# Kernel tuning notes

Measured on AMD Instinct MI355X. Metric: run time of the kernel, lower is better.

Reference implementation:

```python
import jax, jax.numpy as jnp
import numpy as np

N_NODES = 100000
N_EDGES = 1600000
NFEAT, NHID, NCLASS = 128, 64, 40
DROPOUT_P = 0.5


def setup_inputs() -> dict:
    key = jax.random.key(0)
    k1, k2, k3, k4 = jax.random.split(key, 4)
    inputs = jax.random.normal(k1, (N_NODES, NFEAT), dtype=jnp.float32)
    edge_index = jax.random.randint(k2, (2, N_EDGES), 0, N_NODES, dtype=jnp.int64)
    # Glorot-uniform-ish init like torch Linear / PyG GCNConv
    lim1 = float(np.sqrt(6.0 / (NFEAT + NHID)))
    lim2 = float(np.sqrt(6.0 / (NHID + NCLASS)))
    W1 = jax.random.uniform(k3, (NFEAT, NHID), minval=-lim1, maxval=lim1, dtype=jnp.float32)
    W2 = jax.random.uniform(k4, (NHID, NCLASS), minval=-lim2, maxval=lim2, dtype=jnp.float32)
    b1 = jnp.zeros((NHID,), dtype=jnp.float32)
    b2 = jnp.zeros((NCLASS,), dtype=jnp.float32)
    return {"inputs": inputs, "edge_index": edge_index, "W1": W1, "b1": b1, "W2": W2, "b2": b2}


def _gcn_conv(x, W, b, src, dst, norm, n_nodes):
    # PyG GCNConv: out[i] = sum_{j->i} norm_ij * (x W)[j] + b
    xw = x @ W                              # [N, out_dim]
    msg = xw[src] * norm[:, None]           # [E+N, out_dim] gather + scale
    out = jax.ops.segment_sum(msg, dst, num_segments=n_nodes)  # scatter-add
    return out + b


def reference(inputs, edge_index, W1, b1, W2, b2):
    n = inputs.shape[0]
    loops = jnp.arange(n, dtype=edge_index.dtype)
    src = jnp.concatenate([edge_index[0], loops])   # add self-loops
    dst = jnp.concatenate([edge_index[1], loops])
    # symmetric normalization D^{-1/2} (A+I) D^{-1/2}
    deg = jax.ops.segment_sum(jnp.ones_like(src, dtype=inputs.dtype), dst, num_segments=n)
    dis = jnp.where(deg > 0, jax.lax.rsqrt(jnp.maximum(deg, 1.0)), 0.0)
    norm = dis[src] * dis[dst]
    # dropout on inputs (training mode, fixed key for determinism)
    keep = jax.random.bernoulli(jax.random.key(42), 1.0 - DROPOUT_P, inputs.shape)
    x = jnp.where(keep, inputs / (1.0 - DROPOUT_P), 0.0)
    h = jax.nn.relu(_gcn_conv(x, W1, b1, src, dst, norm, n))
    out = _gcn_conv(h, W2, b2, src, dst, norm, n)
    return out
```

## Files before the change

kernel.cpp:

```cpp
#include <hip/hip_runtime.h>

#define NF 128
#define NH 64
#define NC 40
#define BSHIFT 10
#define NB 98
#define BIN_T 8192

typedef __attribute__((ext_vector_type(8))) short short8;
typedef __attribute__((ext_vector_type(4))) float float4v;

__device__ __forceinline__ unsigned rotl32(unsigned v, int s) { return (v << s) | (v >> (32 - s)); }

__device__ __forceinline__ unsigned short f2bf(float f) {
  unsigned u = __float_as_uint(f);
  return (unsigned short)((u + 0x7FFFu + ((u >> 16) & 1u)) >> 16);
}
__device__ __forceinline__ float bf2f(unsigned short b) {
  return __uint_as_float(((unsigned)b) << 16);
}

__device__ __forceinline__ unsigned threefry_bits(unsigned idx) {
  const unsigned k0 = 0u, k1 = 42u;
  const unsigned k2x = 0u ^ 42u ^ 0x1BD11BDAu;
  unsigned x0 = 0u, x1 = idx;
  x0 += k0; x1 += k1;
  x0 += x1; x1 = rotl32(x1, 13); x1 ^= x0;
  x0 += x1; x1 = rotl32(x1, 15); x1 ^= x0;
  x0 += x1; x1 = rotl32(x1, 26); x1 ^= x0;
  x0 += x1; x1 = rotl32(x1, 6);  x1 ^= x0;
  x0 += k1; x1 += k2x + 1u;
  x0 += x1; x1 = rotl32(x1, 17); x1 ^= x0;
  x0 += x1; x1 = rotl32(x1, 29); x1 ^= x0;
  x0 += x1; x1 = rotl32(x1, 16); x1 ^= x0;
  x0 += x1; x1 = rotl32(x1, 24); x1 ^= x0;
  x0 += k2x; x1 += k0 + 2u;
  x0 += x1; x1 = rotl32(x1, 13); x1 ^= x0;
  x0 += x1; x1 = rotl32(x1, 15); x1 ^= x0;
  x0 += x1; x1 = rotl32(x1, 26); x1 ^= x0;
  x0 += x1; x1 = rotl32(x1, 6);  x1 ^= x0;
  x0 += k0; x1 += k1 + 3u;
  x0 += x1; x1 = rotl32(x1, 17); x1 ^= x0;
  x0 += x1; x1 = rotl32(x1, 29); x1 ^= x0;
  x0 += x1; x1 = rotl32(x1, 16); x1 ^= x0;
  x0 += x1; x1 = rotl32(x1, 24); x1 ^= x0;
  x0 += k1; x1 += k2x + 4u;
  x0 += x1; x1 = rotl32(x1, 13); x1 ^= x0;
  x0 += x1; x1 = rotl32(x1, 15); x1 ^= x0;
  x0 += x1; x1 = rotl32(x1, 26); x1 ^= x0;
  x0 += x1; x1 = rotl32(x1, 6);  x1 ^= x0;
  x0 += k2x; x1 += k0 + 5u;
  return x0 ^ x1;
}

__global__ __launch_bounds__(256) void k_prep(const float* __restrict__ W1, const float* __restrict__ W2,
                                              unsigned short* __restrict__ Wt1b, unsigned short* __restrict__ Wt2b) {
  int id = blockIdx.x * 256 + threadIdx.x;
  if (id < NF * NH) {
    int k = id >> 6, c = id & 63;
    Wt1b[c * NF + k] = f2bf(W1[id]);
  } else if (id < NF * NH + 48 * NH) {
    int id2 = id - NF * NH;
    int c = id2 >> 6, k = id2 & 63;
    Wt2b[c * NH + k] = (c < NC) ? f2bf(W2[k * NC + c]) : 0;
  }
}

__global__ __launch_bounds__(256) void k_bhist(const int* __restrict__ dst, int* __restrict__ bcnt, int nE) {
  __shared__ int h[NB];
  int t = threadIdx.x;
  if (t < NB) h[t] = 0;
  __syncthreads();
  int stride = gridDim.x * 256;
  for (int e = blockIdx.x * 256 + t; e < nE; e += stride)
    atomicAdd(&h[dst[e] >> BSHIFT], 1);
  __syncthreads();
  if (t < NB && h[t]) atomicAdd(&bcnt[t], h[t]);
}

__global__ __launch_bounds__(128) void k_bscan(const int* __restrict__ bcnt, int* __restrict__ bbase,
                                               int* __restrict__ gcur, int* __restrict__ rp, int n, int nE) {
  int t = threadIdx.x;
  int v = (t < NB) ? bcnt[t] : 0;
  __shared__ int sh[128];
  sh[t] = v; __syncthreads();
  for (int off = 1; off < 128; off <<= 1) {
    int u = (t >= off) ? sh[t - off] : 0; __syncthreads();
    sh[t] += u; __syncthreads();
  }
  int excl = sh[t] - v;
  if (t < NB) { bbase[t] = excl; gcur[t] = excl; }
  if (t == 0) { bbase[NB] = nE; rp[n] = nE; }
}

__global__ __launch_bounds__(256) void k_bin(const int* __restrict__ src, const int* __restrict__ dst,
                                             int* __restrict__ gcur, unsigned* __restrict__ binned, int nE) {
  __shared__ int h[NB];
  __shared__ int off[NB];
  int t = threadIdx.x;
  int b0 = blockIdx.x * BIN_T;
  int b1 = b0 + BIN_T; if (b1 > nE) b1 = nE;
  if (t < NB) h[t] = 0;
  __syncthreads();
  for (int e = b0 + t; e < b1; e += 256)
    atomicAdd(&h[dst[e] >> BSHIFT], 1);
  __syncthreads();
  if (t < NB && h[t] > 0) off[t] = atomicAdd(&gcur[t], h[t]);
  __syncthreads();
  for (int e = b0 + t; e < b1; e += 256) {
    int s = src[e], d = dst[e];
    int p = atomicAdd(&off[d >> BSHIFT], 1);
    binned[p] = ((unsigned)s << BSHIFT) | (unsigned)(d & ((1 << BSHIFT) - 1));
  }
}

__global__ __launch_bounds__(1024) void k_fillb(const unsigned* __restrict__ binned, const int* __restrict__ bbase,
                                                int* __restrict__ rp, float* __restrict__ dis,
                                                int* __restrict__ csrc, int n) {
  __shared__ int hist[1024];
  __shared__ int sbuf[1024];
  int b = blockIdx.x;
  int base = b << BSHIFT;
  int t = threadIdx.x;
  int lo = bbase[b], hi = bbase[b + 1];
  hist[t] = 0;
  __syncthreads();
  for (int e = lo + t; e < hi; e += 1024)
    atomicAdd(&hist[binned[e] & 1023u], 1);
  __syncthreads();
  int v = hist[t];
  sbuf[t] = v; __syncthreads();
  for (int off = 1; off < 1024; off <<= 1) {
    int u = (t >= off) ? sbuf[t - off] : 0; __syncthreads();
    sbuf[t] += u; __syncthreads();
  }
  int excl = sbuf[t] - v;
  if (base + t < n) {
    rp[base + t] = lo + excl;
    dis[base + t] = rsqrtf((float)(v + 1));
  }
  __syncthreads();
  hist[t] = lo + excl;
  __syncthreads();
  for (int e = lo + t; e < hi; e += 1024) {
    unsigned p = binned[e];
    int pos = atomicAdd(&hist[p & 1023u], 1);
    csrc[pos] = (int)(p >> BSHIFT);
  }
}

__global__ __launch_bounds__(256) void k_xw(const float* __restrict__ x, const unsigned short* __restrict__ Wt1b,
                                            const float* __restrict__ dis, unsigned short* __restrict__ y1b, int n) {
  __shared__ unsigned short Ws[NH * 136];
  __shared__ unsigned short xs[16 * 136];
  int t = threadIdx.x;
  int nodeBase = blockIdx.x * 16;
  for (int id = t; id < NH * 16; id += 256) {
    int c = id >> 4, kc = id & 15;
    *(short8*)&Ws[c * 136 + kc * 8] = *(const short8*)&Wt1b[c * NF + kc * 8];
  }
  {
    int nloc = t >> 4, kbase = (t & 15) * 8;
    int ebase = (nodeBase + nloc) * NF + kbase;
    const float4* xp = (const float4*)x;
    float4 a = xp[(ebase >> 2)];
    float4 b = xp[(ebase >> 2) + 1];
    float v[8] = {a.x, a.y, a.z, a.w, b.x, b.y, b.z, b.w};
#pragma unroll
    for (int q = 0; q < 8; ++q) {
      unsigned idx = (unsigned)(ebase + q);
      bool keep = (threefry_bits(idx) & 0x80000000u) == 0u;
      xs[nloc * 136 + kbase + q] = keep ? f2bf(v[q] * 2.0f) : 0;
    }
  }
  __syncthreads();
  int w = t >> 6, lane = t & 63;
  int m = lane & 15, quad = lane >> 4;
  float4v acc = {0.f, 0.f, 0.f, 0.f};
#pragma unroll
  for (int ks = 0; ks < 4; ++ks) {
    short8 a = *(const short8*)&xs[m * 136 + ks * 32 + quad * 8];
    short8 b = *(const short8*)&Ws[(w * 16 + m) * 136 + ks * 32 + quad * 8];
    acc = __builtin_amdgcn_mfma_f32_16x16x32_bf16(a, b, acc, 0, 0, 0);
  }
#pragma unroll
  for (int r = 0; r < 4; ++r) {
    int node = nodeBase + quad * 4 + r;
    y1b[node * NH + w * 16 + m] = f2bf(acc[r] * dis[node]);
  }
}

#define ACC8(u) \
  a0 += __uint_as_float((u).x << 16); \
  a1 += __uint_as_float((u).x & 0xFFFF0000u); \
  a2 += __uint_as_float((u).y << 16); \
  a3 += __uint_as_float((u).y & 0xFFFF0000u); \
  a4 += __uint_as_float((u).z << 16); \
  a5 += __uint_as_float((u).z & 0xFFFF0000u); \
  a6 += __uint_as_float((u).w << 16); \
  a7 += __uint_as_float((u).w & 0xFFFF0000u);

__device__ __forceinline__ unsigned packbf(float lo, float hi) {
  return (unsigned)f2bf(lo) | ((unsigned)f2bf(hi) << 16);
}

__global__ __launch_bounds__(256) void k_agg1(const unsigned short* __restrict__ y1b, const int* __restrict__ rp,
                                              const int* __restrict__ csrc, const float* __restrict__ dis,
                                              const float* __restrict__ b1, unsigned short* __restrict__ gb, int n) {
  int i = blockIdx.x * 32 + (threadIdx.x >> 3);
  if (i >= n) return;
  int fl = (threadIdx.x & 7) << 3;
  const uint4 us = *(const uint4*)&y1b[(i << 6) + fl];
  float a0 = __uint_as_float(us.x << 16);
  float a1 = __uint_as_float(us.x & 0xFFFF0000u);
  float a2 = __uint_as_float(us.y << 16);
  float a3 = __uint_as_float(us.y & 0xFFFF0000u);
  float a4 = __uint_as_float(us.z << 16);
  float a5 = __uint_as_float(us.z & 0xFFFF0000u);
  float a6 = __uint_as_float(us.w << 16);
  float a7 = __uint_as_float(us.w & 0xFFFF0000u);
  int lo = rp[i], hi = rp[i + 1];
  int e = lo;
  int s0, s1, s2, s3;
  if (e + 4 <= hi) { s0 = csrc[e]; s1 = csrc[e + 1]; s2 = csrc[e + 2]; s3 = csrc[e + 3]; }
  for (; e + 8 <= hi; e += 4) {
    uint4 u0 = *(const uint4*)&y1b[(s0 << 6) + fl];
    uint4 u1 = *(const uint4*)&y1b[(s1 << 6) + fl];
    uint4 u2 = *(const uint4*)&y1b[(s2 << 6) + fl];
    uint4 u3 = *(const uint4*)&y1b[(s3 << 6) + fl];
    s0 = csrc[e + 4]; s1 = csrc[e + 5]; s2 = csrc[e + 6]; s3 = csrc[e + 7];
    ACC8(u0) ACC8(u1) ACC8(u2) ACC8(u3)
  }
  if (e + 4 <= hi) {
    uint4 u0 = *(const uint4*)&y1b[(s0 << 6) + fl];
    uint4 u1 = *(const uint4*)&y1b[(s1 << 6) + fl];
    uint4 u2 = *(const uint4*)&y1b[(s2 << 6) + fl];
    uint4 u3 = *(const uint4*)&y1b[(s3 << 6) + fl];
    ACC8(u0) ACC8(u1) ACC8(u2) ACC8(u3)
    e += 4;
  }
  for (; e < hi; ++e) {
    int s = csrc[e];
    uint4 u = *(const uint4*)&y1b[(s << 6) + fl];
    ACC8(u)
  }
  float di = dis[i];
  float4 bb0 = *(const float4*)&b1[fl];
  float4 bb1 = *(const float4*)&b1[fl + 4];
  uint4 o;
  o.x = packbf(di * fmaxf(fmaf(di, a0, bb0.x), 0.f), di * fmaxf(fmaf(di, a1, bb0.y), 0.f));
  o.y = packbf(di * fmaxf(fmaf(di, a2, bb0.z), 0.f), di * fmaxf(fmaf(di, a3, bb0.w), 0.f));
  o.z = packbf(di * fmaxf(fmaf(di, a4, bb1.x), 0.f), di * fmaxf(fmaf(di, a5, bb1.y), 0.f));
  o.w = packbf(di * fmaxf(fmaf(di, a6, bb1.z), 0.f), di * fmaxf(fmaf(di, a7, bb1.w), 0.f));
  *(uint4*)&gb[(i << 6) + fl] = o;
}

__global__ __launch_bounds__(256) void k_aggg(const unsigned short* __restrict__ gb, const int* __restrict__ rp,
                                              const int* __restrict__ csrc, const float* __restrict__ dis,
                                              unsigned short* __restrict__ ahb, int n) {
  int i = blockIdx.x * 32 + (threadIdx.x >> 3);
  if (i >= n) return;
  int fl = (threadIdx.x & 7) << 3;
  const uint4 us = *(const uint4*)&gb[(i << 6) + fl];
  float a0 = __uint_as_float(us.x << 16);
  float a1 = __uint_as_float(us.x & 0xFFFF0000u);
  float a2 = __uint_as_float(us.y << 16);
  float a3 = __uint_as_float(us.y & 0xFFFF0000u);
  float a4 = __uint_as_float(us.z << 16);
  float a5 = __uint_as_float(us.z & 0xFFFF0000u);
  float a6 = __uint_as_float(us.w << 16);
  float a7 = __uint_as_float(us.w & 0xFFFF0000u);
  int lo = rp[i], hi = rp[i + 1];
  int e = lo;
  int s0, s1, s2, s3;
  if (e + 4 <= hi) { s0 = csrc[e]; s1 = csrc[e + 1]; s2 = csrc[e + 2]; s3 = csrc[e + 3]; }
  for (; e + 8 <= hi; e += 4) {
    uint4 u0 = *(const uint4*)&gb[(s0 << 6) + fl];
    uint4 u1 = *(const uint4*)&gb[(s1 << 6) + fl];
    uint4 u2 = *(const uint4*)&gb[(s2 << 6) + fl];
    uint4 u3 = *(const uint4*)&gb[(s3 << 6) + fl];
    s0 = csrc[e + 4]; s1 = csrc[e + 5]; s2 = csrc[e + 6]; s3 = csrc[e + 7];
    ACC8(u0) ACC8(u1) ACC8(u2) ACC8(u3)
  }
  if (e + 4 <= hi) {
    uint4 u0 = *(const uint4*)&gb[(s0 << 6) + fl];
    uint4 u1 = *(const uint4*)&gb[(s1 << 6) + fl];
    uint4 u2 = *(const uint4*)&gb[(s2 << 6) + fl];
    uint4 u3 = *(const uint4*)&gb[(s3 << 6) + fl];
    ACC8(u0) ACC8(u1) ACC8(u2) ACC8(u3)
    e += 4;
  }
  for (; e < hi; ++e) {
    int s = csrc[e];
    uint4 u = *(const uint4*)&gb[(s << 6) + fl];
    ACC8(u)
  }
  float di = dis[i];
  uint4 o;
  o.x = packbf(di * a0, di * a1);
  o.y = packbf(di * a2, di * a3);
  o.z = packbf(di * a4, di * a5);
  o.w = packbf(di * a6, di * a7);
  *(uint4*)&ahb[(i << 6) + fl] = o;
}

__global__ __launch_bounds__(192) void k_hw2(const unsigned short* __restrict__ ahb, const unsigned short* __restrict__ Wt2b,
                                             const float* __restrict__ b2, float* __restrict__ out, int n) {
  __shared__ unsigned short Ws[48 * 72];
  __shared__ unsigned short xs[16 * 72];
  int t = threadIdx.x;
  int nodeBase = blockIdx.x * 16;
  for (int id = t; id < 48 * 8; id += 192) {
    int c = id >> 3, kc = id & 7;
    *(short8*)&Ws[c * 72 + kc * 8] = *(const short8*)&Wt2b[c * NH + kc * 8];
  }
  if (t < 128) {
    int c = t >> 3, kc = t & 7;
    *(short8*)&xs[c * 72 + kc * 8] = *(const short8*)&ahb[(nodeBase + c) * NH + kc * 8];
  }
  __syncthreads();
  int w = t >> 6, lane = t & 63;
  int m = lane & 15, quad = lane >> 4;
  float4v acc = {0.f, 0.f, 0.f, 0.f};
#pragma unroll
  for (int ks = 0; ks < 2; ++ks) {
    short8 a = *(const short8*)&xs[m * 72 + ks * 32 + quad * 8];
    short8 b = *(const short8*)&Ws[(w * 16 + m) * 72 + ks * 32 + quad * 8];
    acc = __builtin_amdgcn_mfma_f32_16x16x32_bf16(a, b, acc, 0, 0, 0);
  }
  int col = w * 16 + m;
  if (col < NC) {
    float bias = b2[col];
#pragma unroll
    for (int r = 0; r < 4; ++r) {
      int node = nodeBase + quad * 4 + r;
      out[node * NC + col] = acc[r] + bias;
    }
  }
}

extern "C" void kernel_launch(void* const* d_in, const int* in_sizes, int n_in,
                              void* d_out, int out_size, void* d_ws, size_t ws_size,
                              hipStream_t stream) {
  const float* x  = (const float*)d_in[0];
  const int*   ei = (const int*)d_in[1];
  const float* W1 = (const float*)d_in[2];
  const float* b1 = (const float*)d_in[3];
  const float* W2 = (const float*)d_in[4];
  const float* b2 = (const float*)d_in[5];
  float* out = (float*)d_out;
  int n  = in_sizes[0] / NF;
  int nE = in_sizes[1] / 2;
  const int* src = ei;
  const int* dst = ei + nE;

  char* ws = (char*)d_ws;
  float* dis   = (float*)(ws + 0);
  int*   rp    = (int*)(ws + 400000);
  int*   bcnt  = (int*)(ws + 800128);
  int*   bbase = (int*)(ws + 800640);
  int*   gcur  = (int*)(ws + 801152);
  unsigned short* Wt1b = (unsigned short*)(ws + 801664);
  unsigned short* Wt2b = (unsigned short*)(ws + 818048);
  int*   csrc  = (int*)(ws + 824192);
  unsigned short* y1b = (unsigned short*)(ws + 7224192);
  unsigned short* gb  = (unsigned short*)(ws + 20024192);
  unsigned* binned = (unsigned*)(ws + 20024192);
  unsigned short* ahb = y1b;

  hipMemsetAsync(bcnt, 0, NB * 4, stream);

  k_prep <<<(NF * NH + 48 * NH + 255) / 256, 256, 0, stream>>>(W1, W2, Wt1b, Wt2b);
  k_bhist<<<512, 256, 0, stream>>>(dst, bcnt, nE);
  k_bscan<<<1, 128, 0, stream>>>(bcnt, bbase, gcur, rp, n, nE);
  k_bin  <<<(nE + BIN_T - 1) / BIN_T, 256, 0, stream>>>(src, dst, gcur, binned, nE);
  k_fillb<<<NB, 1024, 0, stream>>>(binned, bbase, rp, dis, csrc, n);
  k_xw   <<<n / 16, 256, 0, stream>>>(x, Wt1b, dis, y1b, n);
  k_agg1 <<<(n + 31) / 32, 256, 0, stream>>>(y1b, rp, csrc, dis, b1, gb, n);
  k_aggg <<<(n + 31) / 32, 256, 0, stream>>>(gb, rp, csrc, dis, ahb, n);
  k_hw2  <<<n / 16, 192, 0, stream>>>(ahb, Wt2b, b2, out, n);
}
```

Measured before the change: 248.0 us.

## Split hidden features into four 16-wide column slabs for cache-local gathers

```diff
diff --git a/kernel.cpp b/kernel.cpp
--- a/kernel.cpp
+++ b/kernel.cpp
@@ -186,7 +186,7 @@
 #pragma unroll
   for (int r = 0; r < 4; ++r) {
     int node = nodeBase + quad * 4 + r;
-    y1b[node * NH + w * 16 + m] = f2bf(acc[r] * dis[node]);
+    y1b[((size_t)w * n + node) * 16 + m] = f2bf(acc[r] * dis[node]);
   }
 }
 
@@ -204,107 +204,115 @@
   return (unsigned)f2bf(lo) | ((unsigned)f2bf(hi) << 16);
 }
 
-__global__ __launch_bounds__(256) void k_agg1(const unsigned short* __restrict__ y1b, const int* __restrict__ rp,
+__global__ __launch_bounds__(256) void k_agg1(const unsigned short* __restrict__ y1q, const int* __restrict__ rp,
                                               const int* __restrict__ csrc, const float* __restrict__ dis,
-                                              const float* __restrict__ b1, unsigned short* __restrict__ gb, int n) {
-  int i = blockIdx.x * 32 + (threadIdx.x >> 3);
+                                              const float* __restrict__ b1, unsigned short* __restrict__ gq, int n) {
+  int i = blockIdx.x * 128 + (threadIdx.x >> 1);
   if (i >= n) return;
-  int fl = (threadIdx.x & 7) << 3;
-  const uint4 us = *(const uint4*)&y1b[(i << 6) + fl];
-  float a0 = __uint_as_float(us.x << 16);
-  float a1 = __uint_as_float(us.x & 0xFFFF0000u);
-  float a2 = __uint_as_float(us.y << 16);
-  float a3 = __uint_as_float(us.y & 0xFFFF0000u);
-  float a4 = __uint_as_float(us.z << 16);
-  float a5 = __uint_as_float(us.z & 0xFFFF0000u);
-  float a6 = __uint_as_float(us.w << 16);
-  float a7 = __uint_as_float(us.w & 0xFFFF0000u);
+  int fl = (threadIdx.x & 1) << 3;
   int lo = rp[i], hi = rp[i + 1];
-  int e = lo;
-  int s0, s1, s2, s3;
-  if (e + 4 <= hi) { s0 = csrc[e]; s1 = csrc[e + 1]; s2 = csrc[e + 2]; s3 = csrc[e + 3]; }
-  for (; e + 8 <= hi; e += 4) {
-    uint4 u0 = *(const uint4*)&y1b[(s0 << 6) + fl];
-    uint4 u1 = *(const uint4*)&y1b[(s1 << 6) + fl];
-    uint4 u2 = *(const uint4*)&y1b[(s2 << 6) + fl];
-    uint4 u3 = *(const uint4*)&y1b[(s3 << 6) + fl];
-    s0 = csrc[e + 4]; s1 = csrc[e + 5]; s2 = csrc[e + 6]; s3 = csrc[e + 7];
-    ACC8(u0) ACC8(u1) ACC8(u2) ACC8(u3)
-  }
-  if (e + 4 <= hi) {
-    uint4 u0 = *(const uint4*)&y1b[(s0 << 6) + fl];
-    uint4 u1 = *(const uint4*)&y1b[(s1 << 6) + fl];
-    uint4 u2 = *(const uint4*)&y1b[(s2 << 6) + fl];
-    uint4 u3 = *(const uint4*)&y1b[(s3 << 6) + fl];
-    ACC8(u0) ACC8(u1) ACC8(u2) ACC8(u3)
-    e += 4;
-  }
-  for (; e < hi; ++e) {
-    int s = csrc[e];
-    uint4 u = *(const uint4*)&y1b[(s << 6) + fl];
-    ACC8(u)
-  }
   float di = dis[i];
-  float4 bb0 = *(const float4*)&b1[fl];
-  float4 bb1 = *(const float4*)&b1[fl + 4];
-  uint4 o;
-  o.x = packbf(di * fmaxf(fmaf(di, a0, bb0.x), 0.f), di * fmaxf(fmaf(di, a1, bb0.y), 0.f));
-  o.y = packbf(di * fmaxf(fmaf(di, a2, bb0.z), 0.f), di * fmaxf(fmaf(di, a3, bb0.w), 0.f));
-  o.z = packbf(di * fmaxf(fmaf(di, a4, bb1.x), 0.f), di * fmaxf(fmaf(di, a5, bb1.y), 0.f));
-  o.w = packbf(di * fmaxf(fmaf(di, a6, bb1.z), 0.f), di * fmaxf(fmaf(di, a7, bb1.w), 0.f));
-  *(uint4*)&gb[(i << 6) + fl] = o;
-}
-
-__global__ __launch_bounds__(256) void k_aggg(const unsigned short* __restrict__ gb, const int* __restrict__ rp,
+#pragma unroll 1
+  for (int q = 0; q < 4; ++q) {
+    const unsigned short* base = y1q + (size_t)q * n * 16;
+    const uint4 us = *(const uint4*)&base[i * 16 + fl];
+    float a0 = __uint_as_float(us.x << 16);
+    float a1 = __uint_as_float(us.x & 0xFFFF0000u);
+    float a2 = __uint_as_float(us.y << 16);
+    float a3 = __uint_as_float(us.y & 0xFFFF0000u);
+    float a4 = __uint_as_float(us.z << 16);
+    float a5 = __uint_as_float(us.z & 0xFFFF0000u);
+    float a6 = __uint_as_float(us.w << 16);
+    float a7 = __uint_as_float(us.w & 0xFFFF0000u);
+    int e = lo;
+    int s0, s1, s2, s3;
+    if (e + 4 <= hi) { s0 = csrc[e]; s1 = csrc[e + 1]; s2 = csrc[e + 2]; s3 = csrc[e + 3]; }
+    for (; e + 8 <= hi; e += 4) {
+      uint4 u0 = *(const uint4*)&base[(s0 << 4) + fl];
+      uint4 u1 = *(const uint4*)&base[(s1 << 4) + fl];
+      uint4 u2 = *(const uint4*)&base[(s2 << 4) + fl];
+      uint4 u3 = *(const uint4*)&base[(s3 << 4) + fl];
+      s0 = csrc[e + 4]; s1 = csrc[e + 5]; s2 = csrc[e + 6]; s3 = csrc[e + 7];
+      ACC8(u0) ACC8(u1) ACC8(u2) ACC8(u3)
+    }
+    if (e + 4 <= hi) {
+      uint4 u0 = *(const uint4*)&base[(s0 << 4) + fl];
+      uint4 u1 = *(const uint4*)&base[(s1 << 4) + fl];
+      uint4 u2 = *(const uint4*)&base[(s2 << 4) + fl];
+      uint4 u3 = *(const uint4*)&base[(s3 << 4) + fl];
+      ACC8(u0) ACC8(u1) ACC8(u2) ACC8(u3)
+      e += 4;
+    }
+    for (; e < hi; ++e) {
+      int s = csrc[e];
+      uint4 u = *(const uint4*)&base[(s << 4) + fl];
+      ACC8(u)
+    }
+    float4 bb0 = *(const float4*)&b1[q * 16 + fl];
+    float4 bb1 = *(const float4*)&b1[q * 16 + fl + 4];
+    uint4 o;
+    o.x = packbf(di * fmaxf(fmaf(di, a0, bb0.x), 0.f), di * fmaxf(fmaf(di, a1, bb0.y), 0.f));
+    o.y = packbf(di * fmaxf(fmaf(di, a2, bb0.z), 0.f), di * fmaxf(fmaf(di, a3, bb0.w), 0.f));
+    o.z = packbf(di * fmaxf(fmaf(di, a4, bb1.x), 0.f), di * fmaxf(fmaf(di, a5, bb1.y), 0.f));
+    o.w = packbf(di * fmaxf(fmaf(di, a6, bb1.z), 0.f), di * fmaxf(fmaf(di, a7, bb1.w), 0.f));
+    *(uint4*)&gq[((size_t)q * n + i) * 16 + fl] = o;
+  }
+}
+
+__global__ __launch_bounds__(256) void k_aggg(const unsigned short* __restrict__ gq, const int* __restrict__ rp,
                                               const int* __restrict__ csrc, const float* __restrict__ dis,
-                                              unsigned short* __restrict__ ahb, int n) {
-  int i = blockIdx.x * 32 + (threadIdx.x >> 3);
+                                              unsigned short* __restrict__ ahq, int n) {
+  int i = blockIdx.x * 128 + (threadIdx.x >> 1);
   if (i >= n) return;
-  int fl = (threadIdx.x & 7) << 3;
-  const uint4 us = *(const uint4*)&gb[(i << 6) + fl];
-  float a0 = __uint_as_float(us.x << 16);
-  float a1 = __uint_as_float(us.x & 0xFFFF0000u);
-  float a2 = __uint_as_float(us.y << 16);
-  float a3 = __uint_as_float(us.y & 0xFFFF0000u);
-  float a4 = __uint_as_float(us.z << 16);
-  float a5 = __uint_as_float(us.z & 0xFFFF0000u);
-  float a6 = __uint_as_float(us.w << 16);
-  float a7 = __uint_as_float(us.w & 0xFFFF0000u);
+  int fl = (threadIdx.x & 1) << 3;
   int lo = rp[i], hi = rp[i + 1];
-  int e = lo;
-  int s0, s1, s2, s3;
-  if (e + 4 <= hi) { s0 = csrc[e]; s1 = csrc[e + 1]; s2 = csrc[e + 2]; s3 = csrc[e + 3]; }
-  for (; e + 8 <= hi; e += 4) {
-    uint4 u0 = *(const uint4*)&gb[(s0 << 6) + fl];
-    uint4 u1 = *(const uint4*)&gb[(s1 << 6) + fl];
-    uint4 u2 = *(const uint4*)&gb[(s2 << 6) + fl];
-    uint4 u3 = *(const uint4*)&gb[(s3 << 6) + fl];
-    s0 = csrc[e + 4]; s1 = csrc[e + 5]; s2 = csrc[e + 6]; s3 = csrc[e + 7];
-    ACC8(u0) ACC8(u1) ACC8(u2) ACC8(u3)
-  }
-  if (e + 4 <= hi) {
-    uint4 u0 = *(const uint4*)&gb[(s0 << 6) + fl];
-    uint4 u1 = *(const uint4*)&gb[(s1 << 6) + fl];
-    uint4 u2 = *(const uint4*)&gb[(s2 << 6) + fl];
-    uint4 u3 = *(const uint4*)&gb[(s3 << 6) + fl];
-    ACC8(u0) ACC8(u1) ACC8(u2) ACC8(u3)
-    e += 4;
-  }
-  for (; e < hi; ++e) {
-    int s = csrc[e];
-    uint4 u = *(const uint4*)&gb[(s << 6) + fl];
-    ACC8(u)
-  }
   float di = dis[i];
-  uint4 o;
-  o.x = packbf(di * a0, di * a1);
-  o.y = packbf(di * a2, di * a3);
-  o.z = packbf(di * a4, di * a5);
-  o.w = packbf(di * a6, di * a7);
-  *(uint4*)&ahb[(i << 6) + fl] = o;
-}
-
-__global__ __launch_bounds__(192) void k_hw2(const unsigned short* __restrict__ ahb, const unsigned short* __restrict__ Wt2b,
+#pragma unroll 1
+  for (int q = 0; q < 4; ++q) {
+    const unsigned short* base = gq + (size_t)q * n * 16;
+    const uint4 us = *(const uint4*)&base[i * 16 + fl];
+    float a0 = __uint_as_float(us.x << 16);
+    float a1 = __uint_as_float(us.x & 0xFFFF0000u);
+    float a2 = __uint_as_float(us.y << 16);
+    float a3 = __uint_as_float(us.y & 0xFFFF0000u);
+    float a4 = __uint_as_float(us.z << 16);
+    float a5 = __uint_as_float(us.z & 0xFFFF0000u);
+    float a6 = __uint_as_float(us.w << 16);
+    float a7 = __uint_as_float(us.w & 0xFFFF0000u);
+    int e = lo;
+    int s0, s1, s2, s3;
+    if (e + 4 <= hi) { s0 = csrc[e]; s1 = csrc[e + 1]; s2 = csrc[e + 2]; s3 = csrc[e + 3]; }
+    for (; e + 8 <= hi; e += 4) {
+      uint4 u0 = *(const uint4*)&base[(s0 << 4) + fl];
+      uint4 u1 = *(const uint4*)&base[(s1 << 4) + fl];
+      uint4 u2 = *(const uint4*)&base[(s2 << 4) + fl];
+      uint4 u3 = *(const uint4*)&base[(s3 << 4) + fl];
+      s0 = csrc[e + 4]; s1 = csrc[e + 5]; s2 = csrc[e + 6]; s3 = csrc[e + 7];
+      ACC8(u0) ACC8(u1) ACC8(u2) ACC8(u3)
+    }
+    if (e + 4 <= hi) {
+      uint4 u0 = *(const uint4*)&base[(s0 << 4) + fl];
+      uint4 u1 = *(const uint4*)&base[(s1 << 4) + fl];
+      uint4 u2 = *(const uint4*)&base[(s2 << 4) + fl];
+      uint4 u3 = *(const uint4*)&base[(s3 << 4) + fl];
+      ACC8(u0) ACC8(u1) ACC8(u2) ACC8(u3)
+      e += 4;
+    }
+    for (; e < hi; ++e) {
+      int s = csrc[e];
+      uint4 u = *(const uint4*)&base[(s << 4) + fl];
+      ACC8(u)
+    }
+    uint4 o;
+    o.x = packbf(di * a0, di * a1);
+    o.y = packbf(di * a2, di * a3);
+    o.z = packbf(di * a4, di * a5);
+    o.w = packbf(di * a6, di * a7);
+    *(uint4*)&ahq[((size_t)q * n + i) * 16 + fl] = o;
+  }
+}
+
+__global__ __launch_bounds__(192) void k_hw2(const unsigned short* __restrict__ ahq, const unsigned short* __restrict__ Wt2b,
                                              const float* __restrict__ b2, float* __restrict__ out, int n) {
   __shared__ unsigned short Ws[48 * 72];
   __shared__ unsigned short xs[16 * 72];
@@ -316,7 +324,8 @@
   }
   if (t < 128) {
     int c = t >> 3, kc = t & 7;
-    *(short8*)&xs[c * 72 + kc * 8] = *(const short8*)&ahb[(nodeBase + c) * NH + kc * 8];
+    int q = kc >> 1, h = kc & 1;
+    *(short8*)&xs[c * 72 + kc * 8] = *(const short8*)&ahq[((size_t)q * n + nodeBase + c) * 16 + h * 8];
   }
   __syncthreads();
   int w = t >> 6, lane = t & 63;
@@ -376,7 +385,7 @@
   k_bin  <<<(nE + BIN_T - 1) / BIN_T, 256, 0, stream>>>(src, dst, gcur, binned, nE);
   k_fillb<<<NB, 1024, 0, stream>>>(binned, bbase, rp, dis, csrc, n);
   k_xw   <<<n / 16, 256, 0, stream>>>(x, Wt1b, dis, y1b, n);
-  k_agg1 <<<(n + 31) / 32, 256, 0, stream>>>(y1b, rp, csrc, dis, b1, gb, n);
-  k_aggg <<<(n + 31) / 32, 256, 0, stream>>>(gb, rp, csrc, dis, ahb, n);
+  k_agg1 <<<(n + 127) / 128, 256, 0, stream>>>(y1b, rp, csrc, dis, b1, gb, n);
+  k_aggg <<<(n + 127) / 128, 256, 0, stream>>>(gb, rp, csrc, dis, ahb, n);
   k_hw2  <<<n / 16, 192, 0, stream>>>(ahb, Wt2b, b2, out, n);
 }
```

Result: slower. 305.0 us (+23.0%).

## Drop bucket histogram and scan passes using fixed-stride bucket slots

Applied to the files above, without the earlier changes.

```diff
diff --git a/kernel.cpp b/kernel.cpp
--- a/kernel.cpp
+++ b/kernel.cpp
@@ -6,6 +6,7 @@
 #define BSHIFT 10
 #define NB 98
 #define BIN_T 8192
+#define BSTRIDE 20480
 
 typedef __attribute__((ext_vector_type(8))) short short8;
 typedef __attribute__((ext_vector_type(4))) float float4v;
@@ -53,51 +54,26 @@
   return x0 ^ x1;
 }
 
-__global__ __launch_bounds__(256) void k_prep(const float* __restrict__ W1, const float* __restrict__ W2,
-                                              unsigned short* __restrict__ Wt1b, unsigned short* __restrict__ Wt2b) {
-  int id = blockIdx.x * 256 + threadIdx.x;
-  if (id < NF * NH) {
-    int k = id >> 6, c = id & 63;
-    Wt1b[c * NF + k] = f2bf(W1[id]);
-  } else if (id < NF * NH + 48 * NH) {
-    int id2 = id - NF * NH;
-    int c = id2 >> 6, k = id2 & 63;
-    Wt2b[c * NH + k] = (c < NC) ? f2bf(W2[k * NC + c]) : 0;
-  }
-}
-
-__global__ __launch_bounds__(256) void k_bhist(const int* __restrict__ dst, int* __restrict__ bcnt, int nE) {
-  __shared__ int h[NB];
+__global__ __launch_bounds__(256) void k_bin(const int* __restrict__ src, const int* __restrict__ dst,
+                                             int* __restrict__ gcur, unsigned* __restrict__ binned,
+                                             const float* __restrict__ W1, const float* __restrict__ W2,
+                                             unsigned short* __restrict__ Wt1b, unsigned short* __restrict__ Wt2b,
+                                             int nE, int nbin) {
   int t = threadIdx.x;
-  if (t < NB) h[t] = 0;
-  __syncthreads();
-  int stride = gridDim.x * 256;
-  for (int e = blockIdx.x * 256 + t; e < nE; e += stride)
-    atomicAdd(&h[dst[e] >> BSHIFT], 1);
-  __syncthreads();
-  if (t < NB && h[t]) atomicAdd(&bcnt[t], h[t]);
-}
-
-__global__ __launch_bounds__(128) void k_bscan(const int* __restrict__ bcnt, int* __restrict__ bbase,
-                                               int* __restrict__ gcur, int* __restrict__ rp, int n, int nE) {
-  int t = threadIdx.x;
-  int v = (t < NB) ? bcnt[t] : 0;
-  __shared__ int sh[128];
-  sh[t] = v; __syncthreads();
-  for (int off = 1; off < 128; off <<= 1) {
-    int u = (t >= off) ? sh[t - off] : 0; __syncthreads();
-    sh[t] += u; __syncthreads();
-  }
-  int excl = sh[t] - v;
-  if (t < NB) { bbase[t] = excl; gcur[t] = excl; }
-  if (t == 0) { bbase[NB] = nE; rp[n] = nE; }
-}
-
-__global__ __launch_bounds__(256) void k_bin(const int* __restrict__ src, const int* __restrict__ dst,
-                                             int* __restrict__ gcur, unsigned* __restrict__ binned, int nE) {
+  if (blockIdx.x >= nbin) {
+    int id = (blockIdx.x - nbin) * 256 + t;
+    if (id < NF * NH) {
+      int k = id >> 6, c = id & 63;
+      Wt1b[c * NF + k] = f2bf(W1[id]);
+    } else if (id < NF * NH + 48 * NH) {
+      int id2 = id - NF * NH;
+      int c = id2 >> 6, k = id2 & 63;
+      Wt2b[c * NH + k] = (c < NC) ? f2bf(W2[k * NC + c]) : 0;
+    }
+    return;
+  }
   __shared__ int h[NB];
   __shared__ int off[NB];
-  int t = threadIdx.x;
   int b0 = blockIdx.x * BIN_T;
   int b1 = b0 + BIN_T; if (b1 > nE) b1 = nE;
   if (t < NB) h[t] = 0;
@@ -105,7 +81,7 @@
   for (int e = b0 + t; e < b1; e += 256)
     atomicAdd(&h[dst[e] >> BSHIFT], 1);
   __syncthreads();
-  if (t < NB && h[t] > 0) off[t] = atomicAdd(&gcur[t], h[t]);
+  if (t < NB && h[t] > 0) off[t] = t * BSTRIDE + atomicAdd(&gcur[t], h[t]);
   __syncthreads();
   for (int e = b0 + t; e < b1; e += 256) {
     int s = src[e], d = dst[e];
@@ -114,15 +90,15 @@
   }
 }
 
-__global__ __launch_bounds__(1024) void k_fillb(const unsigned* __restrict__ binned, const int* __restrict__ bbase,
-                                                int* __restrict__ rp, float* __restrict__ dis,
+__global__ __launch_bounds__(1024) void k_fillb(const unsigned* __restrict__ binned, const int* __restrict__ gcur,
+                                                unsigned* __restrict__ rpd, float* __restrict__ dis,
                                                 int* __restrict__ csrc, int n) {
   __shared__ int hist[1024];
   __shared__ int sbuf[1024];
   int b = blockIdx.x;
   int base = b << BSHIFT;
   int t = threadIdx.x;
-  int lo = bbase[b], hi = bbase[b + 1];
+  int lo = b * BSTRIDE, hi = lo + gcur[b];
   hist[t] = 0;
   __syncthreads();
   for (int e = lo + t; e < hi; e += 1024)
@@ -136,7 +112,7 @@
   }
   int excl = sbuf[t] - v;
   if (base + t < n) {
-    rp[base + t] = lo + excl;
+    rpd[base + t] = ((unsigned)(lo + excl) << 11) | (unsigned)v;
     dis[base + t] = rsqrtf((float)(v + 1));
   }
   __syncthreads();
@@ -204,7 +180,7 @@
   return (unsigned)f2bf(lo) | ((unsigned)f2bf(hi) << 16);
 }
 
-__global__ __launch_bounds__(256) void k_agg1(const unsigned short* __restrict__ y1b, const int* __restrict__ rp,
+__global__ __launch_bounds__(256) void k_agg1(const unsigned short* __restrict__ y1b, const unsigned* __restrict__ rpd,
                                               const int* __restrict__ csrc, const float* __restrict__ dis,
                                               const float* __restrict__ b1, unsigned short* __restrict__ gb, int n) {
   int i = blockIdx.x * 32 + (threadIdx.x >> 3);
@@ -219,7 +195,8 @@
   float a5 = __uint_as_float(us.z & 0xFFFF0000u);
   float a6 = __uint_as_float(us.w << 16);
   float a7 = __uint_as_float(us.w & 0xFFFF0000u);
-  int lo = rp[i], hi = rp[i + 1];
+  unsigned rd = rpd[i];
+  int lo = (int)(rd >> 11), hi = lo + (int)(rd & 2047u);
   int e = lo;
   int s0, s1, s2, s3;
   if (e + 4 <= hi) { s0 = csrc[e]; s1 = csrc[e + 1]; s2 = csrc[e + 2]; s3 = csrc[e + 3]; }
@@ -255,7 +232,7 @@
   *(uint4*)&gb[(i << 6) + fl] = o;
 }
 
-__global__ __launch_bounds__(256) void k_aggg(const unsigned short* __restrict__ gb, const int* __restrict__ rp,
+__global__ __launch_bounds__(256) void k_aggg(const unsigned short* __restrict__ gb, const unsigned* __restrict__ rpd,
                                               const int* __restrict__ csrc, const float* __restrict__ dis,
                                               unsigned short* __restrict__ ahb, int n) {
   int i = blockIdx.x * 32 + (threadIdx.x >> 3);
@@ -270,7 +247,8 @@
   float a5 = __uint_as_float(us.z & 0xFFFF0000u);
   float a6 = __uint_as_float(us.w << 16);
   float a7 = __uint_as_float(us.w & 0xFFFF0000u);
-  int lo = rp[i], hi = rp[i + 1];
+  unsigned rd = rpd[i];
+  int lo = (int)(rd >> 11), hi = lo + (int)(rd & 2047u);
   int e = lo;
   int s0, s1, s2, s3;
   if (e + 4 <= hi) { s0 = csrc[e]; s1 = csrc[e + 1]; s2 = csrc[e + 2]; s3 = csrc[e + 3]; }
@@ -355,28 +333,25 @@
   const int* dst = ei + nE;
 
   char* ws = (char*)d_ws;
-  float* dis   = (float*)(ws + 0);
-  int*   rp    = (int*)(ws + 400000);
-  int*   bcnt  = (int*)(ws + 800128);
-  int*   bbase = (int*)(ws + 800640);
-  int*   gcur  = (int*)(ws + 801152);
-  unsigned short* Wt1b = (unsigned short*)(ws + 801664);
-  unsigned short* Wt2b = (unsigned short*)(ws + 818048);
-  int*   csrc  = (int*)(ws + 824192);
-  unsigned short* y1b = (unsigned short*)(ws + 7224192);
-  unsigned short* gb  = (unsigned short*)(ws + 20024192);
-  unsigned* binned = (unsigned*)(ws + 20024192);
+  float*    dis  = (float*)(ws + 0);
+  unsigned* rpd  = (unsigned*)(ws + 400000);
+  int*      gcur = (int*)(ws + 800000);
+  unsigned short* Wt1b = (unsigned short*)(ws + 800512);
+  unsigned short* Wt2b = (unsigned short*)(ws + 816896);
+  int*      csrc = (int*)(ws + 823296);
+  unsigned short* y1b = (unsigned short*)(ws + 8851456);
+  unsigned short* gb  = (unsigned short*)(ws + 21651456);
+  unsigned* binned = (unsigned*)(ws + 21651456);
   unsigned short* ahb = y1b;
 
-  hipMemsetAsync(bcnt, 0, NB * 4, stream);
-
-  k_prep <<<(NF * NH + 48 * NH + 255) / 256, 256, 0, stream>>>(W1, W2, Wt1b, Wt2b);
-  k_bhist<<<512, 256, 0, stream>>>(dst, bcnt, nE);
-  k_bscan<<<1, 128, 0, stream>>>(bcnt, bbase, gcur, rp, n, nE);
-  k_bin  <<<(nE + BIN_T - 1) / BIN_T, 256, 0, stream>>>(src, dst, gcur, binned, nE);
-  k_fillb<<<NB, 1024, 0, stream>>>(binned, bbase, rp, dis, csrc, n);
+  hipMemsetAsync(gcur, 0, NB * 4, stream);
+
+  int nbin = (nE + BIN_T - 1) / BIN_T;
+  int nprep = (NF * NH + 48 * NH + 255) / 256;
+  k_bin  <<<nbin + nprep, 256, 0, stream>>>(src, dst, gcur, binned, W1, W2, Wt1b, Wt2b, nE, nbin);
+  k_fillb<<<NB, 1024, 0, stream>>>(binned, gcur, rpd, dis, csrc, n);
   k_xw   <<<n / 16, 256, 0, stream>>>(x, Wt1b, dis, y1b, n);
-  k_agg1 <<<(n + 31) / 32, 256, 0, stream>>>(y1b, rp, csrc, dis, b1, gb, n);
-  k_aggg <<<(n + 31) / 32, 256, 0, stream>>>(gb, rp, csrc, dis, ahb, n);
+  k_agg1 <<<(n + 31) / 32, 256, 0, stream>>>(y1b, rpd, csrc, dis, b1, gb, n);
+  k_aggg <<<(n + 31) / 32, 256, 0, stream>>>(gb, rpd, csrc, dis, ahb, n);
   k_hw2  <<<n / 16, 192, 0, stream>>>(ahb, Wt2b, b2, out, n);
 }
```

Result: faster. 230.2 us (-7.1%).
